# Kernel optimization log

Measured on AMD Instinct MI355X. Metric: run time of the kernel, lower is better.

## Reference

```python
import jax, jax.numpy as jnp
import numpy as np

N_NODES = 50000
N_EDGES = 600000
N_GRAPHS = 512
D = 128          # in_channels == hidden_channels
L = 4            # num_layers (total GINConv count)
N_CLASSES = 10
BN_EPS = 1e-5


def setup_inputs() -> dict:
    key = jax.random.key(0)
    ks = jax.random.split(key, 12)
    x = jax.random.normal(ks[0], (N_NODES, D), dtype=jnp.float32)
    edge_index = jax.random.randint(ks[1], (2, N_EDGES), 0, N_NODES, dtype=jnp.int64)
    batch = jnp.sort(jax.random.randint(ks[2], (N_NODES,), 0, N_GRAPHS, dtype=jnp.int64))
    s = 1.0 / np.sqrt(D)
    W1 = jax.random.uniform(ks[3], (L, D, D), jnp.float32, -s, s)
    b1 = jax.random.uniform(ks[4], (L, D), jnp.float32, -s, s)
    W2 = jax.random.uniform(ks[5], (L, D, D), jnp.float32, -s, s)
    b2 = jax.random.uniform(ks[6], (L, D), jnp.float32, -s, s)
    eps = jnp.zeros((L,), jnp.float32)            # train_eps=True, init 0
    gamma = jnp.ones((L, D), jnp.float32)
    beta = jnp.zeros((L, D), jnp.float32)
    sl = 1.0 / np.sqrt(D * L)
    Wlin = jax.random.uniform(ks[7], (D * L, N_CLASSES), jnp.float32, -sl, sl)
    blin = jax.random.uniform(ks[8], (N_CLASSES,), jnp.float32, -sl, sl)
    return {"x": x, "edge_index": edge_index, "batch": batch,
            "W1": W1, "b1": b1, "W2": W2, "b2": b2, "eps": eps,
            "gamma": gamma, "beta": beta, "Wlin": Wlin, "blin": blin}


def reference(x, edge_index, batch, W1, b1, W2, b2, eps, gamma, beta, Wlin, blin):
    src, dst = edge_index[0], edge_index[1]
    h = x
    pools = []
    for l in range(L):
        # GINConv: sum-aggregate neighbor features at dst, add (1+eps)*self
        agg = jax.ops.segment_sum(h[src], dst, num_segments=N_NODES)
        z = (1.0 + eps[l]) * h + agg
        # 2-layer MLP
        z = jnp.maximum(z @ W1[l] + b1[l], 0.0) @ W2[l] + b2[l]
        # BatchNorm1d (training mode: batch stats, biased variance)
        mean = jnp.mean(z, axis=0)
        var = jnp.mean(jnp.square(z - mean), axis=0)
        z = (z - mean) * jax.lax.rsqrt(var + BN_EPS) * gamma[l] + beta[l]
        h = jnp.maximum(z, 0.0)
        # global_add_pool per graph
        pools.append(jax.ops.segment_sum(h, batch, num_segments=N_GRAPHS))
    x_cat = jnp.concatenate(pools, axis=1)  # [N_GRAPHS, D*L]
    return x_cat @ Wlin + blin              # dropout = identity (eval)
```

## Files before the change

### kernel.cpp

```cpp
#include <hip/hip_runtime.h>

#define N_NODES 50000
#define N_EDGES 600000
#define N_GRAPHS 512
#define DIM 128
#define NLAYERS 4
#define NCLASSES 10
#define KPS 136

typedef __attribute__((ext_vector_type(8))) short short8;
typedef __attribute__((ext_vector_type(4))) float f32x4;

union Frag { short8 s; uint4 u; };

__device__ inline unsigned short f2bf(float v) {
    union { float f; unsigned u; } c; c.f = v;
    unsigned u = c.u;
    u += 0x7FFFu + ((u >> 16) & 1u);
    return (unsigned short)(u >> 16);
}
__device__ inline float bfu_lo(unsigned u) {
    union { float f; unsigned x; } c; c.x = u << 16; return c.f;
}
__device__ inline float bfu_hi(unsigned u) {
    union { float f; unsigned x; } c; c.x = u & 0xFFFF0000u; return c.f;
}
__device__ inline void addRow(float* acc, const uint4& v) {
    acc[0] += bfu_lo(v.x); acc[1] += bfu_hi(v.x);
    acc[2] += bfu_lo(v.y); acc[3] += bfu_hi(v.y);
    acc[4] += bfu_lo(v.z); acc[5] += bfu_hi(v.z);
    acc[6] += bfu_lo(v.w); acc[7] += bfu_hi(v.w);
}

__global__ __launch_bounds__(256) void hist_kernel(
    const int* __restrict__ dst, int* __restrict__ deg)
{
    int e = blockIdx.x * 256 + threadIdx.x;
    if (e >= N_EDGES) return;
    atomicAdd(&deg[dst[e]], 1);
}

__global__ __launch_bounds__(256) void scan1_kernel(
    const int* __restrict__ deg, int* __restrict__ bsum)
{
    __shared__ int red[256];
    int t = threadIdx.x;
    int i4 = blockIdx.x * 256 + t;
    int s = 0;
    if (i4 < 12500) {
        int4 v = ((const int4*)deg)[i4];
        s = v.x + v.y + v.z + v.w;
    }
    red[t] = s;
    __syncthreads();
    for (int off = 128; off > 0; off >>= 1) {
        if (t < off) red[t] += red[t + off];
        __syncthreads();
    }
    if (t == 0) bsum[blockIdx.x] = red[0];
}

__global__ __launch_bounds__(64) void scan2_kernel(int* __restrict__ bsum)
{
    __shared__ int sh[64];
    int t = threadIdx.x;
    sh[t] = (t < 49) ? bsum[t] : 0;
    __syncthreads();
    if (t == 0) {
        int run = 0;
        for (int i = 0; i < 49; i++) { int v = sh[i]; sh[i] = run; run += v; }
    }
    __syncthreads();
    if (t < 49) bsum[t] = sh[t];
}

__global__ __launch_bounds__(256) void scan3_kernel(
    const int* __restrict__ deg, const int* __restrict__ bsum,
    int* __restrict__ rowptr, int* __restrict__ cursor)
{
    __shared__ int red[256];
    int t = threadIdx.x;
    int i4 = blockIdx.x * 256 + t;
    int4 v = {0, 0, 0, 0};
    if (i4 < 12500) v = ((const int4*)deg)[i4];
    int s = v.x + v.y + v.z + v.w;
    red[t] = s;
    __syncthreads();
    for (int off = 1; off < 256; off <<= 1) {
        int val = (t >= off) ? red[t - off] : 0;
        __syncthreads();
        red[t] += val;
        __syncthreads();
    }
    int run = bsum[blockIdx.x] + (t ? red[t - 1] : 0);
    if (i4 < 12500) {
        int4 rp;
        rp.x = run; run += v.x;
        rp.y = run; run += v.y;
        rp.z = run; run += v.z;
        rp.w = run; run += v.w;
        ((int4*)rowptr)[i4] = rp;
        ((int4*)cursor)[i4] = rp;
    }
    if (blockIdx.x == 0 && t == 0) rowptr[N_NODES] = N_EDGES;
}

__global__ __launch_bounds__(256) void fill_kernel(
    const int* __restrict__ src, const int* __restrict__ dst,
    int* __restrict__ cursor, int* __restrict__ csr)
{
    int e = blockIdx.x * 256 + threadIdx.x;
    if (e >= N_EDGES) return;
    int p = atomicAdd(&cursor[dst[e]], 1);
    csr[p] = src[e];
}

__global__ __launch_bounds__(256) void prep_kernel(
    const int* __restrict__ batch, int* __restrict__ gstart,
    const float* __restrict__ x, unsigned int* __restrict__ xb,
    const float* __restrict__ W1, const float* __restrict__ W2,
    unsigned short* __restrict__ whi, float* __restrict__ stats)
{
    int b = blockIdx.x;
    int t = threadIdx.x;
    if (b < 196) {
        int n = b * 256 + t;
        if (n >= N_NODES) return;
        int bb = batch[n];
        int bp = (n == 0) ? -1 : batch[n - 1];
        for (int g = bp + 1; g <= bb; g++) gstart[g] = n;
        if (n == N_NODES - 1)
            for (int g = bb + 1; g <= N_GRAPHS; g++) gstart[g] = N_NODES;
    } else if (b < 6446) {
        int idx = (b - 196) * 256 + t;
        if (idx >= N_NODES * 32) return;
        float4 v = ((const float4*)x)[idx];
        uint2 o;
        o.x = (unsigned)f2bf(v.x) | ((unsigned)f2bf(v.y) << 16);
        o.y = (unsigned)f2bf(v.z) | ((unsigned)f2bf(v.w) << 16);
        ((uint2*)xb)[idx] = o;
    } else if (b < 6958) {
        int idx = (b - 6446) * 256 + t;
        int f   = idx & 16383;
        int w01 = (idx >> 14) & 1;
        int l   = idx >> 15;
        int j    = f & 7;
        int lane = (f >> 3) & 63;
        int cg   = (f >> 9) & 7;
        int ks   = f >> 12;
        int k = ks * 32 + (lane >> 4) * 8 + j;
        int n = cg * 16 + (lane & 15);
        const float* W = (w01 == 0 ? W1 : W2) + (size_t)l * 16384;
        whi[idx] = f2bf(W[k * 128 + n]);
    } else {
        #pragma unroll
        for (int i = 0; i < 4; i++) stats[i * 256 + t] = 0.f;
    }
}

__global__ __launch_bounds__(256) void gin_layer_kernel(
    const unsigned int* __restrict__ hb,
    const int* __restrict__ rowptr, const int* __restrict__ csr,
    const float* __restrict__ epsP,
    unsigned short* __restrict__ z,
    const unsigned short* __restrict__ whi,
    const float* __restrict__ b1, const float* __restrict__ b2,
    float* __restrict__ stats)
{
    __shared__ unsigned short tpk[64 * KPS];
    __shared__ float sums[1024];
    __shared__ float sqs[1024];

    const int t = threadIdx.x;
    const int lane = t & 63;
    const int w = t >> 6;
    const int wr = w & 1, wc = w >> 1;
    const int l15 = lane & 15, quad = lane >> 4;
    const int base = blockIdx.x * 64;

    {
        const int m = t >> 2;
        const int c = t & 3;
        const int n = base + m;
        const uint4* hb4 = (const uint4*)hb;
        float acc[32];
        #pragma unroll
        for (int i = 0; i < 32; i++) acc[i] = 0.f;
        if (n < N_NODES) {
            const float e1 = 1.0f + epsP[0];
            const uint4* self = hb4 + (size_t)n * 16 + c;
            #pragma unroll
            for (int j = 0; j < 4; j++) {
                uint4 v = self[j * 4];
                float* a = acc + j * 8;
                a[0] = e1 * bfu_lo(v.x); a[1] = e1 * bfu_hi(v.x);
                a[2] = e1 * bfu_lo(v.y); a[3] = e1 * bfu_hi(v.y);
                a[4] = e1 * bfu_lo(v.z); a[5] = e1 * bfu_hi(v.z);
                a[6] = e1 * bfu_lo(v.w); a[7] = e1 * bfu_hi(v.w);
            }
            int beg = rowptr[n], end = rowptr[n + 1];
            int e = beg;
            if (e + 3 < end) {
                int s0 = csr[e], s1 = csr[e + 1], s2 = csr[e + 2], s3 = csr[e + 3];
                while (true) {
                    const uint4* r0 = hb4 + (size_t)s0 * 16 + c;
                    const uint4* r1 = hb4 + (size_t)s1 * 16 + c;
                    const uint4* r2 = hb4 + (size_t)s2 * 16 + c;
                    const uint4* r3 = hb4 + (size_t)s3 * 16 + c;
                    uint4 v00 = r0[0], v01 = r0[4], v02 = r0[8], v03 = r0[12];
                    uint4 v10 = r1[0], v11 = r1[4], v12 = r1[8], v13 = r1[12];
                    uint4 v20 = r2[0], v21 = r2[4], v22 = r2[8], v23 = r2[12];
                    uint4 v30 = r3[0], v31 = r3[4], v32 = r3[8], v33 = r3[12];
                    int en = e + 4;
                    bool more = (en + 3 < end);
                    if (more) {
                        s0 = csr[en]; s1 = csr[en + 1];
                        s2 = csr[en + 2]; s3 = csr[en + 3];
                    }
                    addRow(acc + 0, v00); addRow(acc + 8, v01); addRow(acc + 16, v02); addRow(acc + 24, v03);
                    addRow(acc + 0, v10); addRow(acc + 8, v11); addRow(acc + 16, v12); addRow(acc + 24, v13);
                    addRow(acc + 0, v20); addRow(acc + 8, v21); addRow(acc + 16, v22); addRow(acc + 24, v23);
                    addRow(acc + 0, v30); addRow(acc + 8, v31); addRow(acc + 16, v32); addRow(acc + 24, v33);
                    e = en;
                    if (!more) break;
                }
            }
            for (; e < end; e++) {
                int s0 = csr[e];
                const uint4* r0 = hb4 + (size_t)s0 * 16 + c;
                uint4 a0 = r0[0], a1 = r0[4], a2 = r0[8], a3 = r0[12];
                addRow(acc + 0, a0);  addRow(acc + 8, a1);
                addRow(acc + 16, a2); addRow(acc + 24, a3);
            }
        }
        #pragma unroll
        for (int j = 0; j < 4; j++) {
            union { short8 s; unsigned short u[8]; } pk;
            #pragma unroll
            for (int i = 0; i < 8; i++) pk.u[i] = f2bf(acc[j * 8 + i]);
            *((short8*)&tpk[m * KPS + j * 32 + c * 8]) = pk.s;
        }
    }
    __syncthreads();

    f32x4 acc[2][4];
    #pragma unroll
    for (int s = 0; s < 2; s++)
        #pragma unroll
        for (int i = 0; i < 4; i++) acc[s][i] = (f32x4){0.f, 0.f, 0.f, 0.f};

    const int arow0 = (32 * wr + l15) * KPS;
    const int arow1 = arow0 + 16 * KPS;

    #pragma unroll
    for (int kh = 0; kh < 2; kh++) {
        Frag bf[2][4];
        short8 a0[2], a1[2];
        #pragma unroll
        for (int kk = 0; kk < 2; kk++) {
            int ks = kh * 2 + kk;
            #pragma unroll
            for (int i = 0; i < 4; i++) {
                size_t woff = (size_t)(((ks * 8 + wc * 4 + i) * 64 + lane) * 8);
                bf[kk][i].s = *((const short8*)&whi[woff]);
            }
            a0[kk] = *((const short8*)&tpk[arow0 + ks * 32 + quad * 8]);
            a1[kk] = *((const short8*)&tpk[arow1 + ks * 32 + quad * 8]);
        }
        #pragma unroll
        for (int kk = 0; kk < 2; kk++) {
            #pragma unroll
            for (int i = 0; i < 4; i++) {
                acc[0][i] = __builtin_amdgcn_mfma_f32_16x16x32_bf16(a0[kk], bf[kk][i].s, acc[0][i], 0, 0, 0);
                acc[1][i] = __builtin_amdgcn_mfma_f32_16x16x32_bf16(a1[kk], bf[kk][i].s, acc[1][i], 0, 0, 0);
            }
        }
    }
    __syncthreads();

    #pragma unroll
    for (int i = 0; i < 4; i++) {
        int col = wc * 64 + i * 16 + l15;
        float bb = b1[col];
        #pragma unroll
        for (int s = 0; s < 2; s++) {
            #pragma unroll
            for (int r = 0; r < 4; r++) {
                int m = 32 * wr + 16 * s + quad * 4 + r;
                float v = fmaxf(acc[s][i][r] + bb, 0.f);
                tpk[m * KPS + col] = f2bf(v);
            }
            acc[s][i] = (f32x4){0.f, 0.f, 0.f, 0.f};
        }
    }
    __syncthreads();

    const unsigned short* w2 = whi + 16384;
    #pragma unroll
    for (int kh = 0; kh < 2; kh++) {
        Frag bf[2][4];
        short8 a0[2], a1[2];
        #pragma unroll
        for (int kk = 0; kk < 2; kk++) {
            int ks = kh * 2 + kk;
            #pragma unroll
            for (int i = 0; i < 4; i++) {
                size_t woff = (size_t)(((ks * 8 + wc * 4 + i) * 64 + lane) * 8);
                bf[kk][i].s = *((const short8*)&w2[woff]);
            }
            a0[kk] = *((const short8*)&tpk[arow0 + ks * 32 + quad * 8]);
            a1[kk] = *((const short8*)&tpk[arow1 + ks * 32 + quad * 8]);
        }
        #pragma unroll
        for (int kk = 0; kk < 2; kk++) {
            #pragma unroll
            for (int i = 0; i < 4; i++) {
                acc[0][i] = __builtin_amdgcn_mfma_f32_16x16x32_bf16(a0[kk], bf[kk][i].s, acc[0][i], 0, 0, 0);
                acc[1][i] = __builtin_amdgcn_mfma_f32_16x16x32_bf16(a1[kk], bf[kk][i].s, acc[1][i], 0, 0, 0);
            }
        }
    }
    __syncthreads();

    {
        float colsum[4], colsq[4];
        #pragma unroll
        for (int i = 0; i < 4; i++) {
            int col = wc * 64 + i * 16 + l15;
            float bb = b2[col];
            float su = 0.f, q2 = 0.f;
            #pragma unroll
            for (int s = 0; s < 2; s++) {
                #pragma unroll
                for (int r = 0; r < 4; r++) {
                    int m = 32 * wr + 16 * s + quad * 4 + r;
                    int n = base + m;
                    float v = acc[s][i][r] + bb;
                    tpk[m * KPS + col] = f2bf(v);
                    if (n < N_NODES) { su += v; q2 += v * v; }
                }
            }
            colsum[i] = su; colsq[i] = q2;
        }
        #pragma unroll
        for (int i = 0; i < 4; i++) {
            sums[(w * 4 + i) * 64 + lane] = colsum[i];
            sqs [(w * 4 + i) * 64 + lane] = colsq[i];
        }
    }
    __syncthreads();

    {
        int m2 = t >> 2, c2 = t & 3;
        int n2 = base + m2;
        if (n2 < N_NODES) {
            const uint4* srcp = (const uint4*)(tpk + m2 * KPS);
            uint4* dstp = (uint4*)z + (size_t)n2 * 16;
            #pragma unroll
            for (int j = 0; j < 4; j++) dstp[j * 4 + c2] = srcp[j * 4 + c2];
        }
    }
    if (t < 128) {
        int c = t;
        int wcc = c >> 6, ci = (c >> 4) & 3, cl = c & 15;
        float s = 0.f, q2 = 0.f;
        #pragma unroll
        for (int wrr = 0; wrr < 2; wrr++) {
            int ww = wcc * 2 + wrr;
            #pragma unroll
            for (int u = 0; u < 4; u++) {
                int ln = cl + u * 16;
                s  += sums[(ww * 4 + ci) * 64 + ln];
                q2 += sqs [(ww * 4 + ci) * 64 + ln];
            }
        }
        unsafeAtomicAdd(&stats[c], s);
        unsafeAtomicAdd(&stats[128 + c], q2);
    }
}

__global__ __launch_bounds__(256) void bnpool_kernel(
    const unsigned int* __restrict__ z, const float* __restrict__ stats,
    const float* __restrict__ gamma, const float* __restrict__ beta,
    const int* __restrict__ gstart, unsigned int* __restrict__ hout,
    float* __restrict__ pools, int layer)
{
    __shared__ float red[8][128];
    const int g = blockIdx.x;
    const int t = threadIdx.x;
    const int q = t & 31, r = t >> 5;
    const int beg = gstart[g], end = gstart[g + 1];

    float4 s  = ((const float4*)stats)[q];
    float4 sq = ((const float4*)stats)[32 + q];
    float4 gm = ((const float4*)gamma)[q];
    float4 bt = ((const float4*)beta)[q];
    const float invN = 1.0f / (float)N_NODES;
    float m, vr;
    float4 scl, sh;
    m = s.x * invN; vr = sq.x * invN - m * m; scl.x = gm.x * rsqrtf(vr + 1e-5f); sh.x = bt.x - m * scl.x;
    m = s.y * invN; vr = sq.y * invN - m * m; scl.y = gm.y * rsqrtf(vr + 1e-5f); sh.y = bt.y - m * scl.y;
    m = s.z * invN; vr = sq.z * invN - m * m; scl.z = gm.z * rsqrtf(vr + 1e-5f); sh.z = bt.z - m * scl.z;
    m = s.w * invN; vr = sq.w * invN - m * m; scl.w = gm.w * rsqrtf(vr + 1e-5f); sh.w = bt.w - m * scl.w;

    float4 acc = {0.f, 0.f, 0.f, 0.f};
    for (int n = beg + r; n < end; n += 8) {
        uint2 zp = ((const uint2*)z)[(size_t)n * 32 + q];
        float4 hv;
        hv.x = fmaxf(bfu_lo(zp.x) * scl.x + sh.x, 0.f);
        hv.y = fmaxf(bfu_hi(zp.x) * scl.y + sh.y, 0.f);
        hv.z = fmaxf(bfu_lo(zp.y) * scl.z + sh.z, 0.f);
        hv.w = fmaxf(bfu_hi(zp.y) * scl.w + sh.w, 0.f);
        uint2 p;
        p.x = (unsigned)f2bf(hv.x) | ((unsigned)f2bf(hv.y) << 16);
        p.y = (unsigned)f2bf(hv.z) | ((unsigned)f2bf(hv.w) << 16);
        ((uint2*)hout)[(size_t)n * 32 + q] = p;
        acc.x += hv.x; acc.y += hv.y; acc.z += hv.z; acc.w += hv.w;
    }
    red[r][q * 4 + 0] = acc.x;
    red[r][q * 4 + 1] = acc.y;
    red[r][q * 4 + 2] = acc.z;
    red[r][q * 4 + 3] = acc.w;
    __syncthreads();
    if (t < 128) {
        float sm = 0.f;
        #pragma unroll
        for (int rr = 0; rr < 8; rr++) sm += red[rr][t];
        pools[(size_t)g * (DIM * NLAYERS) + (size_t)layer * DIM + t] = sm;
    }
}

__global__ __launch_bounds__(64) void final_kernel(
    const float* __restrict__ pools, const float* __restrict__ Wlin,
    const float* __restrict__ blin, float* __restrict__ out)
{
    int g = blockIdx.x;
    int lane = threadIdx.x;
    const float* xr = pools + (size_t)g * (DIM * NLAYERS);
    float a[NCLASSES];
    #pragma unroll
    for (int o = 0; o < NCLASSES; o++) a[o] = 0.f;
    for (int kk = 0; kk < DIM * NLAYERS; kk += 64) {
        float xv = xr[kk + lane];
        const float* wr = Wlin + (size_t)(kk + lane) * NCLASSES;
        #pragma unroll
        for (int o = 0; o < NCLASSES; o++) a[o] += xv * wr[o];
    }
    #pragma unroll
    for (int o = 0; o < NCLASSES; o++) {
        float v = a[o];
        #pragma unroll
        for (int off = 32; off > 0; off >>= 1) v += __shfl_down(v, off, 64);
        if (lane == 0) out[(size_t)g * NCLASSES + o] = v + blin[o];
    }
}

extern "C" void kernel_launch(void* const* d_in, const int* in_sizes, int n_in,
                              void* d_out, int out_size, void* d_ws, size_t ws_size,
                              hipStream_t stream)
{
    const float* x     = (const float*)d_in[0];
    const int*   src   = (const int*)d_in[1];
    const int*   dst   = ((const int*)d_in[1]) + N_EDGES;
    const int*   batch = (const int*)d_in[2];
    const float* W1    = (const float*)d_in[3];
    const float* b1    = (const float*)d_in[4];
    const float* W2    = (const float*)d_in[5];
    const float* b2    = (const float*)d_in[6];
    const float* eps   = (const float*)d_in[7];
    const float* gamma = (const float*)d_in[8];
    const float* beta  = (const float*)d_in[9];
    const float* Wlin  = (const float*)d_in[10];
    const float* blin  = (const float*)d_in[11];
    float* out = (float*)d_out;

    char* ws = (char*)d_ws;
    const size_t FEATH = (size_t)N_NODES * DIM * sizeof(unsigned short);
    size_t off = 0;
    unsigned int* buf_h = (unsigned int*)(ws + off); off += FEATH;
    unsigned short* buf_z = (unsigned short*)(ws + off); off += FEATH;
    float* pools  = (float*)(ws + off); off += (size_t)N_GRAPHS * DIM * NLAYERS * sizeof(float);
    float* stats  = (float*)(ws + off); off += (size_t)NLAYERS * 256 * sizeof(float);
    int*   deg    = (int*)(ws + off);   off += (size_t)N_NODES * sizeof(int);
    int*   rowptr = (int*)(ws + off);   off += (size_t)(N_NODES + 1) * sizeof(int) + 12;
    int*   csr    = (int*)(ws + off);   off += (size_t)N_EDGES * sizeof(int);
    int*   gstart = (int*)(ws + off);   off += 2064;
    int*   bsum   = (int*)(ws + off);   off += 208;
    unsigned short* whi = (unsigned short*)(ws + off); off += (size_t)NLAYERS * 2 * 16384 * 2;

    hipMemsetAsync(deg, 0, (size_t)N_NODES * sizeof(int), stream);

    hist_kernel<<<(N_EDGES + 255) / 256, 256, 0, stream>>>(dst, deg);
    scan1_kernel<<<49, 256, 0, stream>>>(deg, bsum);
    scan2_kernel<<<1, 64, 0, stream>>>(bsum);
    scan3_kernel<<<49, 256, 0, stream>>>(deg, bsum, rowptr, deg );
    fill_kernel<<<(N_EDGES + 255) / 256, 256, 0, stream>>>(src, dst, deg, csr);
    prep_kernel<<<6959, 256, 0, stream>>>(batch, gstart, x, buf_h,
                                          W1, W2, whi, stats);

    for (int l = 0; l < NLAYERS; l++) {
        gin_layer_kernel<<<(N_NODES + 63) / 64, 256, 0, stream>>>(
            buf_h, rowptr, csr, eps + l, buf_z,
            whi + (size_t)l * 32768,
            b1 + (size_t)l * DIM, b2 + (size_t)l * DIM,
            stats + (size_t)l * 256);
        bnpool_kernel<<<N_GRAPHS, 256, 0, stream>>>(
            (const unsigned int*)buf_z, stats + (size_t)l * 256,
            gamma + (size_t)l * DIM, beta + (size_t)l * DIM,
            gstart, buf_h, pools, l);
    }
    final_kernel<<<N_GRAPHS, 64, 0, stream>>>(pools, Wlin, blin, out);
}
```

Before: 406.8 us.

## Halve GIN layer tile to 32 nodes and fuse last BN-pool with head

The fused gather+MLP kernel now handles 32 nodes per block instead of 64, with 8 threads per node each gathering two 16-byte chunks. Each wave now does one 16-row MFMA tile, and launch bounds request 5 blocks per CU. This cuts registers and shared memory so more waves can hide gather latency, but the weight fragment loads are now amortised over half as many rows. Separately, the last layer's BN/pool kernel is fused with the final linear head, which drops one launch and the final write of h that nothing reads.

New measurement: 441.0 us. 1.08x slower.

```diff
diff --git a/kernel.cpp b/kernel.cpp
--- a/kernel.cpp
+++ b/kernel.cpp
@@ -158,7 +158,7 @@
     }
 }
 
-__global__ __launch_bounds__(256) void gin_layer_kernel(
+__global__ __launch_bounds__(256, 5) void gin_layer_kernel(
     const unsigned int* __restrict__ hb,
     const int* __restrict__ rowptr, const int* __restrict__ csr,
     const float* __restrict__ epsP,
@@ -167,7 +167,7 @@
     const float* __restrict__ b1, const float* __restrict__ b2,
     float* __restrict__ stats)
 {
-    __shared__ unsigned short tpk[64 * KPS];
+    __shared__ unsigned short tpk[32 * KPS];
     __shared__ float sums[1024];
     __shared__ float sqs[1024];
 
@@ -176,28 +176,28 @@
     const int w = t >> 6;
     const int wr = w & 1, wc = w >> 1;
     const int l15 = lane & 15, quad = lane >> 4;
-    const int base = blockIdx.x * 64;
+    const int base = blockIdx.x * 32;
 
     {
-        const int m = t >> 2;
-        const int c = t & 3;
+        const int m = t >> 3;
+        const int c = t & 7;
         const int n = base + m;
         const uint4* hb4 = (const uint4*)hb;
-        float acc[32];
-        #pragma unroll
-        for (int i = 0; i < 32; i++) acc[i] = 0.f;
+        float acc[16];
+        #pragma unroll
+        for (int i = 0; i < 16; i++) acc[i] = 0.f;
         if (n < N_NODES) {
             const float e1 = 1.0f + epsP[0];
             const uint4* self = hb4 + (size_t)n * 16 + c;
-            #pragma unroll
-            for (int j = 0; j < 4; j++) {
-                uint4 v = self[j * 4];
-                float* a = acc + j * 8;
-                a[0] = e1 * bfu_lo(v.x); a[1] = e1 * bfu_hi(v.x);
-                a[2] = e1 * bfu_lo(v.y); a[3] = e1 * bfu_hi(v.y);
-                a[4] = e1 * bfu_lo(v.z); a[5] = e1 * bfu_hi(v.z);
-                a[6] = e1 * bfu_lo(v.w); a[7] = e1 * bfu_hi(v.w);
-            }
+            uint4 sv0 = self[0], sv1 = self[8];
+            acc[0]  = e1 * bfu_lo(sv0.x); acc[1]  = e1 * bfu_hi(sv0.x);
+            acc[2]  = e1 * bfu_lo(sv0.y); acc[3]  = e1 * bfu_hi(sv0.y);
+            acc[4]  = e1 * bfu_lo(sv0.z); acc[5]  = e1 * bfu_hi(sv0.z);
+            acc[6]  = e1 * bfu_lo(sv0.w); acc[7]  = e1 * bfu_hi(sv0.w);
+            acc[8]  = e1 * bfu_lo(sv1.x); acc[9]  = e1 * bfu_hi(sv1.x);
+            acc[10] = e1 * bfu_lo(sv1.y); acc[11] = e1 * bfu_hi(sv1.y);
+            acc[12] = e1 * bfu_lo(sv1.z); acc[13] = e1 * bfu_hi(sv1.z);
+            acc[14] = e1 * bfu_lo(sv1.w); acc[15] = e1 * bfu_hi(sv1.w);
             int beg = rowptr[n], end = rowptr[n + 1];
             int e = beg;
             if (e + 3 < end) {
@@ -207,20 +207,20 @@
                     const uint4* r1 = hb4 + (size_t)s1 * 16 + c;
                     const uint4* r2 = hb4 + (size_t)s2 * 16 + c;
                     const uint4* r3 = hb4 + (size_t)s3 * 16 + c;
-                    uint4 v00 = r0[0], v01 = r0[4], v02 = r0[8], v03 = r0[12];
-                    uint4 v10 = r1[0], v11 = r1[4], v12 = r1[8], v13 = r1[12];
-                    uint4 v20 = r2[0], v21 = r2[4], v22 = r2[8], v23 = r2[12];
-                    uint4 v30 = r3[0], v31 = r3[4], v32 = r3[8], v33 = r3[12];
+                    uint4 v00 = r0[0], v01 = r0[8];
+                    uint4 v10 = r1[0], v11 = r1[8];
+                    uint4 v20 = r2[0], v21 = r2[8];
+                    uint4 v30 = r3[0], v31 = r3[8];
                     int en = e + 4;
                     bool more = (en + 3 < end);
                     if (more) {
                         s0 = csr[en]; s1 = csr[en + 1];
                         s2 = csr[en + 2]; s3 = csr[en + 3];
                     }
-                    addRow(acc + 0, v00); addRow(acc + 8, v01); addRow(acc + 16, v02); addRow(acc + 24, v03);
-                    addRow(acc + 0, v10); addRow(acc + 8, v11); addRow(acc + 16, v12); addRow(acc + 24, v13);
-                    addRow(acc + 0, v20); addRow(acc + 8, v21); addRow(acc + 16, v22); addRow(acc + 24, v23);
-                    addRow(acc + 0, v30); addRow(acc + 8, v31); addRow(acc + 16, v32); addRow(acc + 24, v33);
+                    addRow(acc + 0, v00); addRow(acc + 8, v01);
+                    addRow(acc + 0, v10); addRow(acc + 8, v11);
+                    addRow(acc + 0, v20); addRow(acc + 8, v21);
+                    addRow(acc + 0, v30); addRow(acc + 8, v31);
                     e = en;
                     if (!more) break;
                 }
@@ -228,34 +228,30 @@
             for (; e < end; e++) {
                 int s0 = csr[e];
                 const uint4* r0 = hb4 + (size_t)s0 * 16 + c;
-                uint4 a0 = r0[0], a1 = r0[4], a2 = r0[8], a3 = r0[12];
-                addRow(acc + 0, a0);  addRow(acc + 8, a1);
-                addRow(acc + 16, a2); addRow(acc + 24, a3);
-            }
-        }
-        #pragma unroll
-        for (int j = 0; j < 4; j++) {
+                uint4 a0 = r0[0], a1 = r0[8];
+                addRow(acc + 0, a0); addRow(acc + 8, a1);
+            }
+        }
+        #pragma unroll
+        for (int j = 0; j < 2; j++) {
             union { short8 s; unsigned short u[8]; } pk;
             #pragma unroll
             for (int i = 0; i < 8; i++) pk.u[i] = f2bf(acc[j * 8 + i]);
-            *((short8*)&tpk[m * KPS + j * 32 + c * 8]) = pk.s;
-        }
-    }
-    __syncthreads();
-
-    f32x4 acc[2][4];
+            *((short8*)&tpk[m * KPS + j * 64 + c * 8]) = pk.s;
+        }
+    }
+    __syncthreads();
+
+    f32x4 acc[4];
     #pragma unroll
-    for (int s = 0; s < 2; s++)
-        #pragma unroll
-        for (int i = 0; i < 4; i++) acc[s][i] = (f32x4){0.f, 0.f, 0.f, 0.f};
-
-    const int arow0 = (32 * wr + l15) * KPS;
-    const int arow1 = arow0 + 16 * KPS;
+    for (int i = 0; i < 4; i++) acc[i] = (f32x4){0.f, 0.f, 0.f, 0.f};
+
+    const int arow = (16 * wr + l15) * KPS;
 
     #pragma unroll
     for (int kh = 0; kh < 2; kh++) {
         Frag bf[2][4];
-        short8 a0[2], a1[2];
+        short8 a0[2];
         #pragma unroll
         for (int kk = 0; kk < 2; kk++) {
             int ks = kh * 2 + kk;
@@ -264,15 +260,13 @@
                 size_t woff = (size_t)(((ks * 8 + wc * 4 + i) * 64 + lane) * 8);
                 bf[kk][i].s = *((const short8*)&whi[woff]);
             }
-            a0[kk] = *((const short8*)&tpk[arow0 + ks * 32 + quad * 8]);
-            a1[kk] = *((const short8*)&tpk[arow1 + ks * 32 + quad * 8]);
+            a0[kk] = *((const short8*)&tpk[arow + ks * 32 + quad * 8]);
         }
         #pragma unroll
         for (int kk = 0; kk < 2; kk++) {
             #pragma unroll
             for (int i = 0; i < 4; i++) {
-                acc[0][i] = __builtin_amdgcn_mfma_f32_16x16x32_bf16(a0[kk], bf[kk][i].s, acc[0][i], 0, 0, 0);
-                acc[1][i] = __builtin_amdgcn_mfma_f32_16x16x32_bf16(a1[kk], bf[kk][i].s, acc[1][i], 0, 0, 0);
+                acc[i] = __builtin_amdgcn_mfma_f32_16x16x32_bf16(a0[kk], bf[kk][i].s, acc[i], 0, 0, 0);
             }
         }
     }
@@ -283,15 +277,12 @@
         int col = wc * 64 + i * 16 + l15;
         float bb = b1[col];
         #pragma unroll
-        for (int s = 0; s < 2; s++) {
-            #pragma unroll
-            for (int r = 0; r < 4; r++) {
-                int m = 32 * wr + 16 * s + quad * 4 + r;
-                float v = fmaxf(acc[s][i][r] + bb, 0.f);
-                tpk[m * KPS + col] = f2bf(v);
-            }
-            acc[s][i] = (f32x4){0.f, 0.f, 0.f, 0.f};
-        }
+        for (int r = 0; r < 4; r++) {
+            int m = 16 * wr + quad * 4 + r;
+            float v = fmaxf(acc[i][r] + bb, 0.f);
+            tpk[m * KPS + col] = f2bf(v);
+        }
+        acc[i] = (f32x4){0.f, 0.f, 0.f, 0.f};
     }
     __syncthreads();
 
@@ -299,7 +290,7 @@
     #pragma unroll
     for (int kh = 0; kh < 2; kh++) {
         Frag bf[2][4];
-        short8 a0[2], a1[2];
+        short8 a0[2];
         #pragma unroll
         for (int kk = 0; kk < 2; kk++) {
             int ks = kh * 2 + kk;
@@ -308,56 +299,46 @@
                 size_t woff = (size_t)(((ks * 8 + wc * 4 + i) * 64 + lane) * 8);
                 bf[kk][i].s = *((const short8*)&w2[woff]);
             }
-            a0[kk] = *((const short8*)&tpk[arow0 + ks * 32 + quad * 8]);
-            a1[kk] = *((const short8*)&tpk[arow1 + ks * 32 + quad * 8]);
+            a0[kk] = *((const short8*)&tpk[arow + ks * 32 + quad * 8]);
         }
         #pragma unroll
         for (int kk = 0; kk < 2; kk++) {
             #pragma unroll
             for (int i = 0; i < 4; i++) {
-                acc[0][i] = __builtin_amdgcn_mfma_f32_16x16x32_bf16(a0[kk], bf[kk][i].s, acc[0][i], 0, 0, 0);
-                acc[1][i] = __builtin_amdgcn_mfma_f32_16x16x32_bf16(a1[kk], bf[kk][i].s, acc[1][i], 0, 0, 0);
+                acc[i] = __builtin_amdgcn_mfma_f32_16x16x32_bf16(a0[kk], bf[kk][i].s, acc[i], 0, 0, 0);
             }
         }
     }
     __syncthreads();
 
     {
-        float colsum[4], colsq[4];
         #pragma unroll
         for (int i = 0; i < 4; i++) {
             int col = wc * 64 + i * 16 + l15;
             float bb = b2[col];
             float su = 0.f, q2 = 0.f;
             #pragma unroll
-            for (int s = 0; s < 2; s++) {
-                #pragma unroll
-                for (int r = 0; r < 4; r++) {
-                    int m = 32 * wr + 16 * s + quad * 4 + r;
-                    int n = base + m;
-                    float v = acc[s][i][r] + bb;
-                    tpk[m * KPS + col] = f2bf(v);
-                    if (n < N_NODES) { su += v; q2 += v * v; }
-                }
-            }
-            colsum[i] = su; colsq[i] = q2;
-        }
-        #pragma unroll
-        for (int i = 0; i < 4; i++) {
-            sums[(w * 4 + i) * 64 + lane] = colsum[i];
-            sqs [(w * 4 + i) * 64 + lane] = colsq[i];
+            for (int r = 0; r < 4; r++) {
+                int m = 16 * wr + quad * 4 + r;
+                int n = base + m;
+                float v = acc[i][r] + bb;
+                tpk[m * KPS + col] = f2bf(v);
+                if (n < N_NODES) { su += v; q2 += v * v; }
+            }
+            sums[(w * 4 + i) * 64 + lane] = su;
+            sqs [(w * 4 + i) * 64 + lane] = q2;
         }
     }
     __syncthreads();
 
     {
-        int m2 = t >> 2, c2 = t & 3;
+        int m2 = t >> 3, c2 = t & 7;
         int n2 = base + m2;
         if (n2 < N_NODES) {
             const uint4* srcp = (const uint4*)(tpk + m2 * KPS);
             uint4* dstp = (uint4*)z + (size_t)n2 * 16;
-            #pragma unroll
-            for (int j = 0; j < 4; j++) dstp[j * 4 + c2] = srcp[j * 4 + c2];
+            dstp[c2]     = srcp[c2];
+            dstp[c2 + 8] = srcp[c2 + 8];
         }
     }
     if (t < 128) {
@@ -430,28 +411,73 @@
     }
 }
 
-__global__ __launch_bounds__(64) void final_kernel(
-    const float* __restrict__ pools, const float* __restrict__ Wlin,
-    const float* __restrict__ blin, float* __restrict__ out)
-{
-    int g = blockIdx.x;
-    int lane = threadIdx.x;
-    const float* xr = pools + (size_t)g * (DIM * NLAYERS);
-    float a[NCLASSES];
-    #pragma unroll
-    for (int o = 0; o < NCLASSES; o++) a[o] = 0.f;
-    for (int kk = 0; kk < DIM * NLAYERS; kk += 64) {
-        float xv = xr[kk + lane];
-        const float* wr = Wlin + (size_t)(kk + lane) * NCLASSES;
-        #pragma unroll
-        for (int o = 0; o < NCLASSES; o++) a[o] += xv * wr[o];
-    }
-    #pragma unroll
-    for (int o = 0; o < NCLASSES; o++) {
-        float v = a[o];
-        #pragma unroll
-        for (int off = 32; off > 0; off >>= 1) v += __shfl_down(v, off, 64);
-        if (lane == 0) out[(size_t)g * NCLASSES + o] = v + blin[o];
+__global__ __launch_bounds__(256) void bnhead_kernel(
+    const unsigned int* __restrict__ z, const float* __restrict__ stats,
+    const float* __restrict__ gamma, const float* __restrict__ beta,
+    const int* __restrict__ gstart, const float* __restrict__ pools,
+    const float* __restrict__ Wlin, const float* __restrict__ blin,
+    float* __restrict__ out)
+{
+    __shared__ float red[8][128];
+    __shared__ float pool3[128];
+    const int g = blockIdx.x;
+    const int t = threadIdx.x;
+    const int q = t & 31, r = t >> 5;
+    const int beg = gstart[g], end = gstart[g + 1];
+
+    float4 s  = ((const float4*)stats)[q];
+    float4 sq = ((const float4*)stats)[32 + q];
+    float4 gm = ((const float4*)gamma)[q];
+    float4 bt = ((const float4*)beta)[q];
+    const float invN = 1.0f / (float)N_NODES;
+    float m, vr;
+    float4 scl, sh;
+    m = s.x * invN; vr = sq.x * invN - m * m; scl.x = gm.x * rsqrtf(vr + 1e-5f); sh.x = bt.x - m * scl.x;
+    m = s.y * invN; vr = sq.y * invN - m * m; scl.y = gm.y * rsqrtf(vr + 1e-5f); sh.y = bt.y - m * scl.y;
+    m = s.z * invN; vr = sq.z * invN - m * m; scl.z = gm.z * rsqrtf(vr + 1e-5f); sh.z = bt.z - m * scl.z;
+    m = s.w * invN; vr = sq.w * invN - m * m; scl.w = gm.w * rsqrtf(vr + 1e-5f); sh.w = bt.w - m * scl.w;
+
+    float4 acc = {0.f, 0.f, 0.f, 0.f};
+    for (int n = beg + r; n < end; n += 8) {
+        uint2 zp = ((const uint2*)z)[(size_t)n * 32 + q];
+        acc.x += fmaxf(bfu_lo(zp.x) * scl.x + sh.x, 0.f);
+        acc.y += fmaxf(bfu_hi(zp.x) * scl.y + sh.y, 0.f);
+        acc.z += fmaxf(bfu_lo(zp.y) * scl.z + sh.z, 0.f);
+        acc.w += fmaxf(bfu_hi(zp.y) * scl.w + sh.w, 0.f);
+    }
+    red[r][q * 4 + 0] = acc.x;
+    red[r][q * 4 + 1] = acc.y;
+    red[r][q * 4 + 2] = acc.z;
+    red[r][q * 4 + 3] = acc.w;
+    __syncthreads();
+    if (t < 128) {
+        float sm = 0.f;
+        #pragma unroll
+        for (int rr = 0; rr < 8; rr++) sm += red[rr][t];
+        pool3[t] = sm;
+    }
+    __syncthreads();
+
+    if (t < 64) {
+        const int lane = t;
+        const float* xr = pools + (size_t)g * (DIM * NLAYERS);
+        float a[NCLASSES];
+        #pragma unroll
+        for (int o = 0; o < NCLASSES; o++) a[o] = 0.f;
+        #pragma unroll
+        for (int kk = 0; kk < DIM * NLAYERS; kk += 64) {
+            float xv = (kk < 3 * DIM) ? xr[kk + lane] : pool3[kk - 3 * DIM + lane];
+            const float* wrow = Wlin + (size_t)(kk + lane) * NCLASSES;
+            #pragma unroll
+            for (int o = 0; o < NCLASSES; o++) a[o] += xv * wrow[o];
+        }
+        #pragma unroll
+        for (int o = 0; o < NCLASSES; o++) {
+            float v = a[o];
+            #pragma unroll
+            for (int off = 32; off > 0; off >>= 1) v += __shfl_down(v, off, 64);
+            if (lane == 0) out[(size_t)g * NCLASSES + o] = v + blin[o];
+        }
     }
 }
 
@@ -499,15 +525,20 @@
                                           W1, W2, whi, stats);
 
     for (int l = 0; l < NLAYERS; l++) {
-        gin_layer_kernel<<<(N_NODES + 63) / 64, 256, 0, stream>>>(
+        gin_layer_kernel<<<(N_NODES + 31) / 32, 256, 0, stream>>>(
             buf_h, rowptr, csr, eps + l, buf_z,
             whi + (size_t)l * 32768,
             b1 + (size_t)l * DIM, b2 + (size_t)l * DIM,
             stats + (size_t)l * 256);
-        bnpool_kernel<<<N_GRAPHS, 256, 0, stream>>>(
-            (const unsigned int*)buf_z, stats + (size_t)l * 256,
-            gamma + (size_t)l * DIM, beta + (size_t)l * DIM,
-            gstart, buf_h, pools, l);
-    }
-    final_kernel<<<N_GRAPHS, 64, 0, stream>>>(pools, Wlin, blin, out);
-}
+        if (l < NLAYERS - 1) {
+            bnpool_kernel<<<N_GRAPHS, 256, 0, stream>>>(
+                (const unsigned int*)buf_z, stats + (size_t)l * 256,
+                gamma + (size_t)l * DIM, beta + (size_t)l * DIM,
+                gstart, buf_h, pools, l);
+        }
+    }
+    bnhead_kernel<<<N_GRAPHS, 256, 0, stream>>>(
+        (const unsigned int*)buf_z, stats + (size_t)(NLAYERS - 1) * 256,
+        gamma + (size_t)(NLAYERS - 1) * DIM, beta + (size_t)(NLAYERS - 1) * DIM,
+        gstart, pools, Wlin, blin, out);
+}
```

## Sort nodes by in-degree for balanced aggregation; fuse last BN-pool with head

Applied to the files above, without the earlier changes.

Builds a per-launch counting sort of nodes by in-degree (bins capped at 63) and has the GIN layer kernel process nodes in that permuted order, so each 64-node block gathers neighbours of similar count, cutting divergence and load imbalance. Outputs are scattered back to original node positions. The final layer's BN/ReLU/pool is fused with the linear head, which skips writing h for the last layer and drops one launch. It adds two small kernels plus extra preprocessing, and gives up the locality of neighbouring node IDs in the gather and scatter.

After: 398.8 us. 2.0% less time.

```diff
diff --git a/kernel.cpp b/kernel.cpp
--- a/kernel.cpp
+++ b/kernel.cpp
@@ -60,10 +60,12 @@
     if (t == 0) bsum[blockIdx.x] = red[0];
 }
 
-__global__ __launch_bounds__(64) void scan2_kernel(int* __restrict__ bsum)
+__global__ __launch_bounds__(64) void scan2_kernel(int* __restrict__ bsum,
+                                                   int* __restrict__ dbins)
 {
     __shared__ int sh[64];
     int t = threadIdx.x;
+    dbins[t] = 0;
     sh[t] = (t < 49) ? bsum[t] : 0;
     __syncthreads();
     if (t == 0) {
@@ -76,9 +78,11 @@
 
 __global__ __launch_bounds__(256) void scan3_kernel(
     const int* __restrict__ deg, const int* __restrict__ bsum,
-    int* __restrict__ rowptr, int* __restrict__ cursor)
+    int* __restrict__ rowptr, int* __restrict__ cursor,
+    int* __restrict__ dbins)
 {
     __shared__ int red[256];
+    __shared__ int lh[64];
     int t = threadIdx.x;
     int i4 = blockIdx.x * 256 + t;
     int4 v = {0, 0, 0, 0};
@@ -103,6 +107,48 @@
         ((int4*)cursor)[i4] = rp;
     }
     if (blockIdx.x == 0 && t == 0) rowptr[N_NODES] = N_EDGES;
+
+    if (t < 64) lh[t] = 0;
+    __syncthreads();
+    if (i4 < 12500) {
+        atomicAdd(&lh[min(v.x, 63)], 1);
+        atomicAdd(&lh[min(v.y, 63)], 1);
+        atomicAdd(&lh[min(v.z, 63)], 1);
+        atomicAdd(&lh[min(v.w, 63)], 1);
+    }
+    __syncthreads();
+    if (t < 64 && lh[t]) atomicAdd(&dbins[t], lh[t]);
+}
+
+__global__ __launch_bounds__(64) void dscan_kernel(
+    const int* __restrict__ dbins, int* __restrict__ dcur)
+{
+    if (threadIdx.x == 0) {
+        int run = 0;
+        for (int i = 0; i < 64; i++) { dcur[i] = run; run += dbins[i]; }
+    }
+}
+
+__global__ __launch_bounds__(256) void dperm_kernel(
+    const int* __restrict__ rowptr, int* __restrict__ dcur,
+    int* __restrict__ perm)
+{
+    __shared__ int lh[64];
+    int t = threadIdx.x;
+    int n = blockIdx.x * 256 + t;
+    bool valid = (n < N_NODES);
+    int b = 0, r = 0;
+    if (t < 64) lh[t] = 0;
+    __syncthreads();
+    if (valid) {
+        int d = rowptr[n + 1] - rowptr[n];
+        b = min(d, 63);
+        r = atomicAdd(&lh[b], 1);
+    }
+    __syncthreads();
+    if (t < 64) lh[t] = atomicAdd(&dcur[t], lh[t]);
+    __syncthreads();
+    if (valid) perm[lh[b] + r] = n;
 }
 
 __global__ __launch_bounds__(256) void fill_kernel(
@@ -161,6 +207,7 @@
 __global__ __launch_bounds__(256) void gin_layer_kernel(
     const unsigned int* __restrict__ hb,
     const int* __restrict__ rowptr, const int* __restrict__ csr,
+    const int* __restrict__ perm,
     const float* __restrict__ epsP,
     unsigned short* __restrict__ z,
     const unsigned short* __restrict__ whi,
@@ -181,7 +228,8 @@
     {
         const int m = t >> 2;
         const int c = t & 3;
-        const int n = base + m;
+        const int idx = base + m;
+        const int n = (idx < N_NODES) ? perm[idx] : N_NODES;
         const uint4* hb4 = (const uint4*)hb;
         float acc[32];
         #pragma unroll
@@ -352,8 +400,9 @@
 
     {
         int m2 = t >> 2, c2 = t & 3;
-        int n2 = base + m2;
-        if (n2 < N_NODES) {
+        int idx2 = base + m2;
+        if (idx2 < N_NODES) {
+            int n2 = perm[idx2];
             const uint4* srcp = (const uint4*)(tpk + m2 * KPS);
             uint4* dstp = (uint4*)z + (size_t)n2 * 16;
             #pragma unroll
@@ -430,28 +479,73 @@
     }
 }
 
-__global__ __launch_bounds__(64) void final_kernel(
-    const float* __restrict__ pools, const float* __restrict__ Wlin,
-    const float* __restrict__ blin, float* __restrict__ out)
-{
-    int g = blockIdx.x;
-    int lane = threadIdx.x;
-    const float* xr = pools + (size_t)g * (DIM * NLAYERS);
-    float a[NCLASSES];
-    #pragma unroll
-    for (int o = 0; o < NCLASSES; o++) a[o] = 0.f;
-    for (int kk = 0; kk < DIM * NLAYERS; kk += 64) {
-        float xv = xr[kk + lane];
-        const float* wr = Wlin + (size_t)(kk + lane) * NCLASSES;
-        #pragma unroll
-        for (int o = 0; o < NCLASSES; o++) a[o] += xv * wr[o];
-    }
-    #pragma unroll
-    for (int o = 0; o < NCLASSES; o++) {
-        float v = a[o];
-        #pragma unroll
-        for (int off = 32; off > 0; off >>= 1) v += __shfl_down(v, off, 64);
-        if (lane == 0) out[(size_t)g * NCLASSES + o] = v + blin[o];
+__global__ __launch_bounds__(256) void bnhead_kernel(
+    const unsigned int* __restrict__ z, const float* __restrict__ stats,
+    const float* __restrict__ gamma, const float* __restrict__ beta,
+    const int* __restrict__ gstart, const float* __restrict__ pools,
+    const float* __restrict__ Wlin, const float* __restrict__ blin,
+    float* __restrict__ out)
+{
+    __shared__ float red[8][128];
+    __shared__ float pool3[128];
+    const int g = blockIdx.x;
+    const int t = threadIdx.x;
+    const int q = t & 31, r = t >> 5;
+    const int beg = gstart[g], end = gstart[g + 1];
+
+    float4 s  = ((const float4*)stats)[q];
+    float4 sq = ((const float4*)stats)[32 + q];
+    float4 gm = ((const float4*)gamma)[q];
+    float4 bt = ((const float4*)beta)[q];
+    const float invN = 1.0f / (float)N_NODES;
+    float m, vr;
+    float4 scl, sh;
+    m = s.x * invN; vr = sq.x * invN - m * m; scl.x = gm.x * rsqrtf(vr + 1e-5f); sh.x = bt.x - m * scl.x;
+    m = s.y * invN; vr = sq.y * invN - m * m; scl.y = gm.y * rsqrtf(vr + 1e-5f); sh.y = bt.y - m * scl.y;
+    m = s.z * invN; vr = sq.z * invN - m * m; scl.z = gm.z * rsqrtf(vr + 1e-5f); sh.z = bt.z - m * scl.z;
+    m = s.w * invN; vr = sq.w * invN - m * m; scl.w = gm.w * rsqrtf(vr + 1e-5f); sh.w = bt.w - m * scl.w;
+
+    float4 acc = {0.f, 0.f, 0.f, 0.f};
+    for (int n = beg + r; n < end; n += 8) {
+        uint2 zp = ((const uint2*)z)[(size_t)n * 32 + q];
+        acc.x += fmaxf(bfu_lo(zp.x) * scl.x + sh.x, 0.f);
+        acc.y += fmaxf(bfu_hi(zp.x) * scl.y + sh.y, 0.f);
+        acc.z += fmaxf(bfu_lo(zp.y) * scl.z + sh.z, 0.f);
+        acc.w += fmaxf(bfu_hi(zp.y) * scl.w + sh.w, 0.f);
+    }
+    red[r][q * 4 + 0] = acc.x;
+    red[r][q * 4 + 1] = acc.y;
+    red[r][q * 4 + 2] = acc.z;
+    red[r][q * 4 + 3] = acc.w;
+    __syncthreads();
+    if (t < 128) {
+        float sm = 0.f;
+        #pragma unroll
+        for (int rr = 0; rr < 8; rr++) sm += red[rr][t];
+        pool3[t] = sm;
+    }
+    __syncthreads();
+
+    if (t < 64) {
+        const int lane = t;
+        const float* xr = pools + (size_t)g * (DIM * NLAYERS);
+        float a[NCLASSES];
+        #pragma unroll
+        for (int o = 0; o < NCLASSES; o++) a[o] = 0.f;
+        #pragma unroll
+        for (int kk = 0; kk < DIM * NLAYERS; kk += 64) {
+            float xv = (kk < 3 * DIM) ? xr[kk + lane] : pool3[kk - 3 * DIM + lane];
+            const float* wrow = Wlin + (size_t)(kk + lane) * NCLASSES;
+            #pragma unroll
+            for (int o = 0; o < NCLASSES; o++) a[o] += xv * wrow[o];
+        }
+        #pragma unroll
+        for (int o = 0; o < NCLASSES; o++) {
+            float v = a[o];
+            #pragma unroll
+            for (int off = 32; off > 0; off >>= 1) v += __shfl_down(v, off, 64);
+            if (lane == 0) out[(size_t)g * NCLASSES + o] = v + blin[o];
+        }
     }
 }
 
@@ -487,27 +581,37 @@
     int*   gstart = (int*)(ws + off);   off += 2064;
     int*   bsum   = (int*)(ws + off);   off += 208;
     unsigned short* whi = (unsigned short*)(ws + off); off += (size_t)NLAYERS * 2 * 16384 * 2;
+    int*   dbins  = (int*)(ws + off);   off += 256;
+    int*   dcur   = (int*)(ws + off);   off += 256;
+    int*   perm   = (int*)(ws + off);   off += (size_t)N_NODES * sizeof(int);
 
     hipMemsetAsync(deg, 0, (size_t)N_NODES * sizeof(int), stream);
 
     hist_kernel<<<(N_EDGES + 255) / 256, 256, 0, stream>>>(dst, deg);
     scan1_kernel<<<49, 256, 0, stream>>>(deg, bsum);
-    scan2_kernel<<<1, 64, 0, stream>>>(bsum);
-    scan3_kernel<<<49, 256, 0, stream>>>(deg, bsum, rowptr, deg );
+    scan2_kernel<<<1, 64, 0, stream>>>(bsum, dbins);
+    scan3_kernel<<<49, 256, 0, stream>>>(deg, bsum, rowptr, deg , dbins);
     fill_kernel<<<(N_EDGES + 255) / 256, 256, 0, stream>>>(src, dst, deg, csr);
+    dscan_kernel<<<1, 64, 0, stream>>>(dbins, dcur);
+    dperm_kernel<<<196, 256, 0, stream>>>(rowptr, dcur, perm);
     prep_kernel<<<6959, 256, 0, stream>>>(batch, gstart, x, buf_h,
                                           W1, W2, whi, stats);
 
     for (int l = 0; l < NLAYERS; l++) {
         gin_layer_kernel<<<(N_NODES + 63) / 64, 256, 0, stream>>>(
-            buf_h, rowptr, csr, eps + l, buf_z,
+            buf_h, rowptr, csr, perm, eps + l, buf_z,
             whi + (size_t)l * 32768,
             b1 + (size_t)l * DIM, b2 + (size_t)l * DIM,
             stats + (size_t)l * 256);
-        bnpool_kernel<<<N_GRAPHS, 256, 0, stream>>>(
-            (const unsigned int*)buf_z, stats + (size_t)l * 256,
-            gamma + (size_t)l * DIM, beta + (size_t)l * DIM,
-            gstart, buf_h, pools, l);
-    }
-    final_kernel<<<N_GRAPHS, 64, 0, stream>>>(pools, Wlin, blin, out);
-}
+        if (l < NLAYERS - 1) {
+            bnpool_kernel<<<N_GRAPHS, 256, 0, stream>>>(
+                (const unsigned int*)buf_z, stats + (size_t)l * 256,
+                gamma + (size_t)l * DIM, beta + (size_t)l * DIM,
+                gstart, buf_h, pools, l);
+        }
+    }
+    bnhead_kernel<<<N_GRAPHS, 256, 0, stream>>>(
+        (const unsigned int*)buf_z, stats + (size_t)(NLAYERS - 1) * 256,
+        gamma + (size_t)(NLAYERS - 1) * DIM, beta + (size_t)(NLAYERS - 1) * DIM,
+        gstart, pools, Wlin, blin, out);
+}
```
